# Optimization experiments

Hardware: AMD Instinct MI355X
Metric: run time of the kernel (lower is better)

The kernel has to match this reference:

```python
import jax, jax.numpy as jnp
import numpy as np

HIDDEN = 768
HEADS = 12
ORDERS = 3
NEG = -1e9


def setup_inputs() -> dict:
    key = jax.random.key(0)
    ks = jax.random.split(key, 16)
    B, N = 8, 512
    s = 0.02
    inp = {
        "v": jax.random.normal(ks[0], (B, N, HIDDEN), jnp.float32),
        "k": jax.random.normal(ks[1], (B, N, HIDDEN), jnp.float32),
        "q": jax.random.normal(ks[2], (B, N, HIDDEN), jnp.float32),
        "masks": jax.random.bernoulli(ks[3], 0.1, (ORDERS, B, 1, N, N)),
        "tau": 1,
        "training": 0,
        "Wv": jax.random.normal(ks[4], (HIDDEN, HIDDEN), jnp.float32) * s,
        "bv": jnp.zeros((HIDDEN,), jnp.float32),
        "Wk": jax.random.normal(ks[5], (HIDDEN, HIDDEN), jnp.float32) * s,
        "bk": jnp.zeros((HIDDEN,), jnp.float32),
        "Wq": jax.random.normal(ks[6], (HIDDEN, HIDDEN), jnp.float32) * s,
        "bq": jnp.zeros((HIDDEN,), jnp.float32),
        "Wm": jax.random.normal(ks[7], (HIDDEN, HIDDEN), jnp.float32) * s,
        "bm": jnp.zeros((HIDDEN,), jnp.float32),
        "pool_w": jax.random.normal(ks[8], (HIDDEN, 1), jnp.float32) * s,
        "pool_b": jnp.zeros((1,), jnp.float32),
        "mlp_w1": jax.random.normal(ks[9], (HIDDEN, HIDDEN // 2), jnp.float32) * s,
        "mlp_w2": jax.random.normal(ks[10], (HIDDEN // 2, ORDERS), jnp.float32) * s,
        "mlp_b2": jnp.zeros((ORDERS,), jnp.float32),
    }
    return inp


def _soft_routing(x, pool_w, pool_b, mlp_w1, mlp_w2, mlp_b2):
    # pooling='fc': masked attention pooling over sequence, then 2-layer MLP + softmax
    pad = (jnp.sum(jnp.abs(x), axis=-1) == 0)[:, :, None]        # [B, N, 1]
    scores = x @ pool_w + pool_b                                  # [B, N, 1]
    scores = jnp.where(pad, NEG, scores)
    scores = jax.nn.softmax(scores, axis=1)
    pooled = jnp.sum(x * scores, axis=1)                          # [B, HIDDEN]
    logits = jax.nn.relu(pooled @ mlp_w1) @ mlp_w2 + mlp_b2       # [B, L]
    return jax.nn.softmax(logits, axis=-1)


def reference(v, k, q, masks, tau, training, Wv, bv, Wk, bk, Wq, bq, Wm, bm,
              pool_w, pool_b, mlp_w1, mlp_w2, mlp_b2):
    B, N, _ = q.shape
    dk = HIDDEN // HEADS
    alphas = _soft_routing(v, pool_w, pool_b, mlp_w1, mlp_w2, mlp_b2)  # [B, L]

    def split_heads(x):
        return x.reshape(B, N, HEADS, dk).transpose(0, 2, 1, 3)  # [B, H, N, dk]

    vh = split_heads(v @ Wv + bv)
    kh = split_heads(k @ Wk + bk)
    qh = split_heads(q @ Wq + bq)

    scores = jnp.einsum('bhnd,bhmd->bhnm', qh, kh) / jnp.sqrt(jnp.float32(dk))
    # masks: [L, B, 1, N, N] broadcast over heads -> att_list [L, B, H, N, N]
    masked = jnp.where(masks[:, :, :, :, :], NEG, scores[None])
    att_list = jax.nn.softmax(masked, axis=-1)                    # [L, B, H, N, N]
    att_map = jnp.einsum('bl,lbhnm->bhnm', alphas, att_list)
    atted = jnp.einsum('bhnm,bhmd->bhnd', att_map, vh)
    atted = atted.transpose(0, 2, 1, 3).reshape(B, N, HIDDEN)
    return atted @ Wm + bm
```

## Files before the change

kernel.cpp:

```cpp
#include <hip/hip_runtime.h>
#include <hip/hip_bf16.h>
#include <stdint.h>


typedef __bf16 bf16x8 __attribute__((ext_vector_type(8)));
typedef float f32x4 __attribute__((ext_vector_type(4)));

#define NEGV -1e9f

__device__ __forceinline__ float b2f(unsigned short h) {
    union { unsigned int u; float f; } x; x.u = ((unsigned int)h) << 16; return x.f;
}
__device__ __forceinline__ unsigned short f2b(float f) {
    union { float f; unsigned int u; } x; x.f = f;
    unsigned int u = x.u + 0x7FFFu + ((x.u >> 16) & 1u);
    return (unsigned short)(u >> 16);
}
__device__ __forceinline__ unsigned int packbf(unsigned int u0, unsigned int u1) {
    unsigned int r0 = (u0 + 0x7FFFu + ((u0 >> 16) & 1u)) >> 16;
    unsigned int r1 = (u1 + 0x7FFFu + ((u1 >> 16) & 1u)) & 0xFFFF0000u;
    return r0 | r1;
}
__device__ __forceinline__ uint4 load8bf(const void* base, size_t elemOff, int isF32) {
    if (!isF32) return *(const uint4*)((const unsigned short*)base + elemOff);
    const uint4* f = (const uint4*)((const float*)base + elemOff);
    uint4 a = f[0], b = f[1];
    uint4 r;
    r.x = packbf(a.x, a.y);
    r.y = packbf(a.z, a.w);
    r.z = packbf(b.x, b.y);
    r.w = packbf(b.z, b.w);
    return r;
}
__device__ __forceinline__ float loadF(const void* p, int idx, int isF32) {
    return isF32 ? ((const float*)p)[idx] : b2f(((const unsigned short*)p)[idx]);
}
__device__ __forceinline__ bf16x8 u2b(uint4 u) {
    union { uint4 a; bf16x8 b; } x; x.a = u; return x.b;
}

__global__ void sniff_kernel(const unsigned int* __restrict__ mp,
                             const unsigned int* __restrict__ vp,
                             const unsigned int* __restrict__ wp,
                             int* __restrict__ flags)
{
    __shared__ int oki, oku, okf, badv, badw;
    if (threadIdx.x == 0) { oki = 1; oku = 1; okf = 1; badv = 0; badw = 0; }
    __syncthreads();
    int li = 1, lu = 1, lf = 1, bv = 0, bw = 0;
    for (int i = threadIdx.x; i < 16384; i += 256) {
        unsigned int w = mp[i];
        if (w > 1u) li = 0;
        if (w & 0xFEFEFEFEu) lu = 0;
        if (w != 0u && w != 0x3F800000u) lf = 0;
    }
    for (int i = threadIdx.x; i < 8192; i += 256) {
        unsigned int w = vp[i];
        float f0 = b2f((unsigned short)(w & 0xFFFF));
        float f1 = b2f((unsigned short)(w >> 16));
        if (!(fabsf(f0) < 1e4f) || !(fabsf(f1) < 1e4f)) bv = 1;
        w = wp[i];
        f0 = b2f((unsigned short)(w & 0xFFFF));
        f1 = b2f((unsigned short)(w >> 16));
        if (!(fabsf(f0) < 1e4f) || !(fabsf(f1) < 1e4f)) bw = 1;
    }
    if (!li) atomicAnd(&oki, 0);
    if (!lu) atomicAnd(&oku, 0);
    if (!lf) atomicAnd(&okf, 0);
    if (bv) atomicOr(&badv, 1);
    if (bw) atomicOr(&badw, 1);
    __syncthreads();
    if (threadIdx.x == 0) {
        flags[0] = oki ? 0 : (oku ? 1 : (okf ? 2 : 3));
        flags[1] = badv;
        flags[2] = badw;
    }
}

__global__ __launch_bounds__(256) void conv_act_kernel(
        const void* __restrict__ v, const void* __restrict__ k,
        const void* __restrict__ q, const int* __restrict__ flags,
        unsigned short* __restrict__ vb, unsigned short* __restrict__ kb,
        unsigned short* __restrict__ qb)
{
    const int dtV = flags[1];
    const int which = blockIdx.y;
    const void* src = (which == 0) ? v : (which == 1) ? k : q;
    unsigned short* dst = (which == 0) ? vb : (which == 1) ? kb : qb;
    size_t off = ((size_t)blockIdx.x * 256 + threadIdx.x) * 8;
    uint4 r = load8bf(src, off, dtV);
    *(uint4*)(dst + off) = r;
}

__global__ __launch_bounds__(256) void conv_wt_kernel(
        const void* __restrict__ W0, const void* __restrict__ W1,
        const void* __restrict__ W2, const void* __restrict__ W3,
        const int* __restrict__ flags,
        unsigned short* __restrict__ T0, unsigned short* __restrict__ T1,
        unsigned short* __restrict__ T2, unsigned short* __restrict__ T3)
{
    __shared__ unsigned short tile[64][65];
    const int t = threadIdx.x;
    const int dtW = flags[2];
    const int which = blockIdx.y;
    const void* W = (which == 0) ? W0 : (which == 1) ? W1 : (which == 2) ? W2 : W3;
    unsigned short* T = (which == 0) ? T0 : (which == 1) ? T1 : (which == 2) ? T2 : T3;
    const int tk = (blockIdx.x / 12) << 6;
    const int tn = (blockIdx.x % 12) << 6;
    #pragma unroll
    for (int i = 0; i < 16; i++) {
        int idx = (i << 8) + t;
        int r = idx >> 6, c = idx & 63;
        tile[r][c] = f2b(loadF(W, (tk + r) * 768 + tn + c, dtW));
    }
    __syncthreads();
    #pragma unroll
    for (int i = 0; i < 16; i++) {
        int idx = (i << 8) + t;
        int rn = idx >> 6, ck = idx & 63;
        T[(size_t)(tn + rn) * 768 + tk + ck] = tile[ck][rn];
    }
}

__global__ __launch_bounds__(256) void pack_kernel(
        const void* __restrict__ masks, const int* __restrict__ flags,
        unsigned int* __restrict__ pm)
{
    __shared__ unsigned char flg[32 * 512];
    const int t = threadIdx.x;
    const int mode = flags[0];
    const size_t e0 = (size_t)blockIdx.x * (32 * 512);
    if (mode == 0 || mode == 2) {
        const uint4* p = (const uint4*)((const unsigned int*)masks + e0);
        for (int i = t; i < 4096; i += 256) {
            uint4 u = p[i];
            int base = i << 2;
            flg[base + 0] = u.x ? 1 : 0;
            flg[base + 1] = u.y ? 1 : 0;
            flg[base + 2] = u.z ? 1 : 0;
            flg[base + 3] = u.w ? 1 : 0;
        }
    } else if (mode == 1) {
        const uint4* p = (const uint4*)((const unsigned char*)masks + e0);
        for (int i = t; i < 1024; i += 256) {
            uint4 u = p[i];
            unsigned int uu[4] = {u.x, u.y, u.z, u.w};
            int base = i << 4;
            #pragma unroll
            for (int k2 = 0; k2 < 4; k2++)
                #pragma unroll
                for (int bb = 0; bb < 4; bb++)
                    flg[base + k2 * 4 + bb] = ((uu[k2] >> (bb * 8)) & 0xFFu) ? 1 : 0;
        }
    } else {
        const uint4* p = (const uint4*)((const unsigned short*)masks + e0);
        for (int i = t; i < 2048; i += 256) {
            uint4 u = p[i];
            unsigned int uu[4] = {u.x, u.y, u.z, u.w};
            int base = i << 3;
            #pragma unroll
            for (int k2 = 0; k2 < 4; k2++) {
                flg[base + k2 * 2 + 0] = (uu[k2] & 0xFFFFu) ? 1 : 0;
                flg[base + k2 * 2 + 1] = (uu[k2] >> 16) ? 1 : 0;
            }
        }
    }
    __syncthreads();
    for (int widx = t; widx < 512; widx += 256) {
        int rl = widx >> 4, lm = widx & 15;
        unsigned int bits = 0;
        #pragma unroll
        for (int g = 0; g < 32; g++)
            bits |= ((unsigned int)(flg[rl * 512 + (g << 4) + lm] & 1)) << g;
        pm[(size_t)blockIdx.x * 512 + widx] = bits;
    }
}

__global__ __launch_bounds__(256) void route_score_kernel(
        const unsigned short* __restrict__ vb, const void* __restrict__ pool_w,
        const void* __restrict__ pool_b, const int* __restrict__ flags,
        float* __restrict__ scores)
{
    __shared__ float pw[768];
    const int t = threadIdx.x;
    const int b = blockIdx.x >> 3, ch = blockIdx.x & 7;
    const int dtW = flags[2];
    for (int d = t; d < 768; d += 256) pw[d] = loadF(pool_w, d, dtW);
    __syncthreads();
    const int r = t >> 2, c4 = t & 3;
    const int n = (ch << 6) + r;
    const unsigned int* vr = (const unsigned int*)vb + ((size_t)(b * 512 + n)) * 384;
    float dot = 0.f, asum = 0.f;
    for (int j = 0; j < 96; j++) {
        int p = c4 + (j << 2);
        unsigned int u = vr[p];
        float f0 = b2f((unsigned short)(u & 0xFFFF));
        float f1 = b2f((unsigned short)(u >> 16));
        asum += fabsf(f0) + fabsf(f1);
        dot += f0 * pw[2 * p] + f1 * pw[2 * p + 1];
    }
    dot += __shfl_xor(dot, 1); dot += __shfl_xor(dot, 2);
    asum += __shfl_xor(asum, 1); asum += __shfl_xor(asum, 2);
    if (c4 == 0)
        scores[b * 512 + n] = (asum == 0.f) ? NEGV : dot + loadF(pool_b, 0, dtW);
}

__global__ __launch_bounds__(512) void route_softmax_kernel(
        const float* __restrict__ scores, float* __restrict__ scs)
{
    __shared__ float red[8];
    const int t = threadIdx.x, b = blockIdx.x;
    float scv = scores[b * 512 + t];
    float mx = scv;
    #pragma unroll
    for (int off = 1; off < 64; off <<= 1) mx = fmaxf(mx, __shfl_xor(mx, off));
    if ((t & 63) == 0) red[t >> 6] = mx;
    __syncthreads();
    float M = red[0];
    #pragma unroll
    for (int i = 1; i < 8; i++) M = fmaxf(M, red[i]);
    float e = __expf(scv - M);
    __syncthreads();
    float sm = e;
    #pragma unroll
    for (int off = 1; off < 64; off <<= 1) sm += __shfl_xor(sm, off);
    if ((t & 63) == 0) red[t >> 6] = sm;
    __syncthreads();
    float SS = 0.f;
    #pragma unroll
    for (int i = 0; i < 8; i++) SS += red[i];
    scs[b * 512 + t] = e / SS;
}

__global__ __launch_bounds__(256) void route_pool_kernel(
        const unsigned short* __restrict__ vbuf, const int* __restrict__ flags,
        const float* __restrict__ scs, float* __restrict__ ppart)
{
    __shared__ float ps[64];
    const int t = threadIdx.x;
    const int ch = blockIdx.x, b = blockIdx.y;
    if (t < 64) ps[t] = scs[b * 512 + (ch << 6) + t];
    __syncthreads();
    const int d0 = t * 3;
    float a0 = 0.f, a1 = 0.f, a2 = 0.f;
    const unsigned short* vp = vbuf + ((size_t)(b * 512 + (ch << 6))) * 768 + d0;
    #pragma unroll 4
    for (int r = 0; r < 64; r++) {
        float p = ps[r];
        a0 += b2f(vp[0]) * p; a1 += b2f(vp[1]) * p; a2 += b2f(vp[2]) * p;
        vp += 768;
    }
    float* o = ppart + ((size_t)(b * 8 + ch)) * 768 + d0;
    o[0] = a0; o[1] = a1; o[2] = a2;
}

__global__ __launch_bounds__(256) void route_hid_kernel(
        const void* __restrict__ w1, const void* __restrict__ w2,
        const int* __restrict__ flags, const float* __restrict__ ppart,
        float* __restrict__ plog)
{
    __shared__ float pool[768];
    __shared__ float red[4][32];
    const int t = threadIdx.x;
    const int jc = blockIdx.x, b = blockIdx.y;
    const int dtW = flags[2];
    for (int d = t; d < 768; d += 256) {
        float a = 0.f;
        #pragma unroll
        for (int c = 0; c < 8; c++) a += ppart[((size_t)(b * 8 + c)) * 768 + d];
        pool[d] = a;
    }
    __syncthreads();
    const int jo = (t & 3) << 3;
    const int dr = t >> 2;
    float acc[8];
    #pragma unroll
    for (int j = 0; j < 8; j++) acc[j] = 0.f;
    for (int it = 0; it < 12; it++) {
        int d = (it << 6) + dr;
        float pv = pool[d];
        size_t off = (size_t)d * 384 + (jc << 5) + jo;
        if (!dtW) {
            uint4 u = *(const uint4*)((const unsigned short*)w1 + off);
            unsigned int uu[4] = {u.x, u.y, u.z, u.w};
            #pragma unroll
            for (int j2 = 0; j2 < 4; j2++) {
                acc[2 * j2]     += pv * b2f((unsigned short)(uu[j2] & 0xFFFF));
                acc[2 * j2 + 1] += pv * b2f((unsigned short)(uu[j2] >> 16));
            }
        } else {
            const float4* f = (const float4*)((const float*)w1 + off);
            float4 u0 = f[0], u1 = f[1];
            acc[0] += pv * u0.x; acc[1] += pv * u0.y;
            acc[2] += pv * u0.z; acc[3] += pv * u0.w;
            acc[4] += pv * u1.x; acc[5] += pv * u1.y;
            acc[6] += pv * u1.z; acc[7] += pv * u1.w;
        }
    }
    #pragma unroll
    for (int off = 4; off < 64; off <<= 1)
        #pragma unroll
        for (int j = 0; j < 8; j++) acc[j] += __shfl_xor(acc[j], off);
    const int w = t >> 6, lane = t & 63;
    if (lane < 4) {
        #pragma unroll
        for (int j = 0; j < 8; j++) red[w][lane * 8 + j] = acc[j];
    }
    __syncthreads();
    if (t < 32) {
        float h = red[0][t] + red[1][t] + red[2][t] + red[3][t];
        h = fmaxf(h, 0.f);
        int jg = (jc << 5) + t;
        float l0 = h * loadF(w2, jg * 3 + 0, dtW);
        float l1 = h * loadF(w2, jg * 3 + 1, dtW);
        float l2 = h * loadF(w2, jg * 3 + 2, dtW);
        #pragma unroll
        for (int off = 1; off < 32; off <<= 1) {
            l0 += __shfl_xor(l0, off);
            l1 += __shfl_xor(l1, off);
            l2 += __shfl_xor(l2, off);
        }
        if (t == 0) {
            float* o = plog + ((size_t)(b * 12 + jc)) * 3;
            o[0] = l0; o[1] = l1; o[2] = l2;
        }
    }
}

__global__ __launch_bounds__(64) void route_alpha_kernel(
        const void* __restrict__ b2, const int* __restrict__ flags,
        const float* __restrict__ plog, float* __restrict__ alphas)
{
    const int t = threadIdx.x, b = blockIdx.x;
    if (t == 0) {
        const int dtW = flags[2];
        float lg[3];
        #pragma unroll
        for (int l = 0; l < 3; l++) {
            float a = loadF(b2, l, dtW);
            for (int jc = 0; jc < 12; jc++) a += plog[((size_t)(b * 12 + jc)) * 3 + l];
            lg[l] = a;
        }
        float mm = fmaxf(lg[0], fmaxf(lg[1], lg[2]));
        float e0 = __expf(lg[0] - mm), e1 = __expf(lg[1] - mm), e2 = __expf(lg[2] - mm);
        float ss = e0 + e1 + e2;
        alphas[b * 3 + 0] = e0 / ss;
        alphas[b * 3 + 1] = e1 / ss;
        alphas[b * 3 + 2] = e2 / ss;
    }
}

__global__ __launch_bounds__(256) void gemm3_kernel(
        const unsigned short* __restrict__ X0, const unsigned short* __restrict__ X1,
        const unsigned short* __restrict__ X2,
        const unsigned short* __restrict__ W0, const unsigned short* __restrict__ W1,
        const unsigned short* __restrict__ W2,
        const void* __restrict__ bias0, const void* __restrict__ bias1,
        const void* __restrict__ bias2,
        const int* __restrict__ flags,
        void* __restrict__ dst0, void* __restrict__ dst1, void* __restrict__ dst2,
        int m0, int m1, int m2)
{
    __shared__ unsigned short smem[8192];
    unsigned short* At = smem;
    unsigned short* Bt = smem + 4096;
    const int t = threadIdx.x;
    const int which = blockIdx.y;
    const unsigned short* X  = (which == 0) ? X0 : (which == 1) ? X1 : X2;
    const unsigned short* WT = (which == 0) ? W0 : (which == 1) ? W1 : W2;
    const void* bias = (which == 0) ? bias0 : (which == 1) ? bias1 : bias2;
    void* dst = (which == 0) ? dst0 : (which == 1) ? dst1 : dst2;
    const int mode = (which == 0) ? m0 : (which == 1) ? m1 : m2;

    const int id = blockIdx.x;
    const int bx = id >> 6, by = id & 63;
    const int row0 = by << 6, col0 = bx << 6;
    const int w = t >> 6, lane = t & 63, quad = lane >> 4, lm = lane & 15;
    const int r0 = t >> 3, c0 = (t & 7) << 3;
    const int wr0 = r0 * 64 + (c0 ^ ((r0 & 7) << 3));
    const int dtW = flags[2];
    const int dtOut = flags[1];

    const unsigned short* xp  = X  + (size_t)(row0 + r0) * 768 + c0;
    const unsigned short* xp2 = xp + 32 * 768;
    const unsigned short* wp  = WT + (size_t)(col0 + r0) * 768 + c0;
    const unsigned short* wp2 = wp + 32 * 768;

    uint4 a0 = *(const uint4*)xp,  a1 = *(const uint4*)xp2;
    uint4 g0 = *(const uint4*)wp,  g1 = *(const uint4*)wp2;

    f32x4 acc[4];
    #pragma unroll
    for (int i = 0; i < 4; i++) acc[i] = (f32x4){0.f, 0.f, 0.f, 0.f};

    const int am = (w << 4) + lm;
    const int abase = am * 64, akey = (am & 7) << 3;

    for (int k0 = 0;;) {
        __syncthreads();
        *(uint4*)&At[wr0] = a0;        *(uint4*)&At[wr0 + 2048] = a1;
        *(uint4*)&Bt[wr0] = g0;        *(uint4*)&Bt[wr0 + 2048] = g1;
        __syncthreads();
        k0 += 64;
        if (k0 < 768) {
            a0 = *(const uint4*)(xp + k0);  a1 = *(const uint4*)(xp2 + k0);
            g0 = *(const uint4*)(wp + k0);  g1 = *(const uint4*)(wp2 + k0);
        }
        #pragma unroll
        for (int ks = 0; ks < 2; ks++) {
            int ko = (quad << 3) + (ks << 5);
            bf16x8 afr = *(const bf16x8*)&At[abase + (ko ^ akey)];
            #pragma unroll
            for (int t4 = 0; t4 < 4; t4++) {
                int bn = (t4 << 4) + lm;
                bf16x8 bfr = *(const bf16x8*)&Bt[bn * 64 + (ko ^ ((bn & 7) << 3))];
                acc[t4] = __builtin_amdgcn_mfma_f32_16x16x32_bf16(afr, bfr, acc[t4], 0, 0, 0);
            }
        }
        if (k0 >= 768) break;
    }

    if (mode == 1 && dtOut) {
        #pragma unroll
        for (int t4 = 0; t4 < 4; t4++) {
            int col = col0 + (t4 << 4) + lm;
            float bsv = loadF(bias, col, dtW);
            #pragma unroll
            for (int rg = 0; rg < 4; rg++) {
                int row = row0 + (w << 4) + (quad << 2) + rg;
                ((float*)dst)[(size_t)row * 768 + col] = acc[t4][rg] + bsv;
            }
        }
        return;
    }

    __syncthreads();
    #pragma unroll
    for (int t4 = 0; t4 < 4; t4++) {
        int colL = (t4 << 4) + lm;
        float bsv = loadF(bias, col0 + colL, dtW);
        #pragma unroll
        for (int rg = 0; rg < 4; rg++) {
            int rowL = (w << 4) + (quad << 2) + rg;
            unsigned short hv = f2b(acc[t4][rg] + bsv);
            if (mode == 2) smem[colL * 72 + rowL] = hv;
            else           smem[rowL * 72 + colL] = hv;
        }
    }
    __syncthreads();
    const int g = t >> 2, cc = (t & 3) << 4;
    uint4 o0 = *(const uint4*)&smem[g * 72 + cc];
    uint4 o1 = *(const uint4*)&smem[g * 72 + cc + 8];
    unsigned short* o;
    if (mode == 0) {
        int b = row0 >> 9, n0b = row0 & 511, h = col0 >> 6;
        o = (unsigned short*)dst + ((size_t)(b * 12 + h) * 512 + n0b + g) * 64 + cc;
    } else if (mode == 2) {
        int b = row0 >> 9, n0b = row0 & 511, h = col0 >> 6;
        o = (unsigned short*)dst + ((size_t)(b * 12 + h) * 64 + g) * 512 + n0b + cc;
    } else {
        o = (unsigned short*)dst + (size_t)(row0 + g) * 768 + col0 + cc;
    }
    *(uint4*)o = o0;
    *(uint4*)(o + 8) = o1;
}

__global__ __launch_bounds__(256) void attn_kernel(
        const unsigned short* __restrict__ qh, const unsigned short* __restrict__ kh,
        const unsigned short* __restrict__ vT, const unsigned int* __restrict__ pm,
        const float* __restrict__ alphas, unsigned short* __restrict__ atted)
{
    __shared__ unsigned short P[16 * 512];
    __shared__ float Zp[4][16][3];
    __shared__ unsigned short Ost[16 * 72];
    const int t = threadIdx.x;
    const int w = t >> 6, lane = t & 63, quad = lane >> 4, lm = lane & 15;
    const int id = blockIdx.x;
    const int bh = id % 96, qb = id / 96;
    const int b = bh / 12, h = bh % 12;
    const int n0 = qb << 4;

    const unsigned short* qrow = qh + ((size_t)(bh * 512 + n0 + lm)) * 64 + (quad << 3);
    bf16x8 qa0 = *(const bf16x8*)qrow;
    bf16x8 qa1 = *(const bf16x8*)(qrow + 32);

    const unsigned short* kb0 = kh + ((size_t)(bh * 512 + (w << 7) + lm)) * 64 + (quad << 3);
    uint4 kv[16];
    #pragma unroll
    for (int nt = 0; nt < 8; nt++) {
        const unsigned short* kr = kb0 + nt * (16 * 64);
        kv[2 * nt]     = *(const uint4*)kr;
        kv[2 * nt + 1] = *(const uint4*)(kr + 32);
    }
    f32x4 acc[8];
    #pragma unroll
    for (int i = 0; i < 8; i++) acc[i] = (f32x4){0.f, 0.f, 0.f, 0.f};
    #pragma unroll
    for (int nt = 0; nt < 8; nt++) {
        acc[nt] = __builtin_amdgcn_mfma_f32_16x16x32_bf16(qa0, u2b(kv[2 * nt]), acc[nt], 0, 0, 0);
        acc[nt] = __builtin_amdgcn_mfma_f32_16x16x32_bf16(qa1, u2b(kv[2 * nt + 1]), acc[nt], 0, 0, 0);
    }

    float al[3];
    #pragma unroll
    for (int l = 0; l < 3; l++) al[l] = alphas[b * 3 + l];

    #pragma unroll
    for (int nt = 0; nt < 8; nt++)
        #pragma unroll
        for (int rg = 0; rg < 4; rg++)
            acc[nt][rg] = __expf(acc[nt][rg] * 0.125f);

    unsigned int mk[4][3];
    #pragma unroll
    for (int rg = 0; rg < 4; rg++)
        #pragma unroll
        for (int l = 0; l < 3; l++)
            mk[rg][l] = pm[((size_t)((l << 3) + b) * 512 + n0 + (quad << 2) + rg) * 16 + lm];

    #pragma unroll
    for (int rg = 0; rg < 4; rg++) {
        float z0 = 0.f, z1 = 0.f, z2 = 0.f;
        #pragma unroll
        for (int nt = 0; nt < 8; nt++) {
            int g = (w << 3) + nt;
            float e = acc[nt][rg];
            if (!((mk[rg][0] >> g) & 1)) z0 += e;
            if (!((mk[rg][1] >> g) & 1)) z1 += e;
            if (!((mk[rg][2] >> g) & 1)) z2 += e;
        }
        #pragma unroll
        for (int off = 1; off < 16; off <<= 1) {
            z0 += __shfl_xor(z0, off);
            z1 += __shfl_xor(z1, off);
            z2 += __shfl_xor(z2, off);
        }
        if (lm == 0) {
            int row = (quad << 2) + rg;
            Zp[w][row][0] = z0; Zp[w][row][1] = z1; Zp[w][row][2] = z2;
        }
    }
    __syncthreads();

    #pragma unroll
    for (int rg = 0; rg < 4; rg++) {
        int row = (quad << 2) + rg;
        float coef[3]; float addu = 0.f;
        #pragma unroll
        for (int l = 0; l < 3; l++) {
            float Z = Zp[0][row][l] + Zp[1][row][l] + Zp[2][row][l] + Zp[3][row][l];
            if (Z > 0.f) coef[l] = al[l] / Z;
            else { coef[l] = 0.f; addu += al[l] * (1.0f / 512.0f); }
        }
        #pragma unroll
        for (int nt = 0; nt < 8; nt++) {
            int g = (w << 3) + nt;
            float p = addu;
            float e = acc[nt][rg];
            if (!((mk[rg][0] >> g) & 1)) p += coef[0] * e;
            if (!((mk[rg][1] >> g) & 1)) p += coef[1] * e;
            if (!((mk[rg][2] >> g) & 1)) p += coef[2] * e;
            int c = (g << 4) + lm;
            int chunk = c >> 3, j = c & 7;
            P[row * 512 + (((chunk ^ (row & 7))) << 3) + j] = f2b(p);
        }
    }
    __syncthreads();

    f32x4 accO = (f32x4){0.f, 0.f, 0.f, 0.f};
    const unsigned short* vb = vT + ((size_t)(bh * 64 + (w << 4) + lm)) * 512 + (quad << 3);
    #pragma unroll
    for (int ks = 0; ks < 16; ks++) {
        bf16x8 pa = *(const bf16x8*)&P[lm * 512 + ((((ks << 2) + quad) ^ (lm & 7)) << 3)];
        bf16x8 vf = *(const bf16x8*)(vb + (ks << 5));
        accO = __builtin_amdgcn_mfma_f32_16x16x32_bf16(pa, vf, accO, 0, 0, 0);
    }
    #pragma unroll
    for (int rg = 0; rg < 4; rg++)
        Ost[((quad << 2) + rg) * 72 + (w << 4) + lm] = f2b(accO[rg]);
    __syncthreads();
    const int r2 = t >> 4, c4 = t & 15;
    uint2 val = *(const uint2*)&Ost[r2 * 72 + (c4 << 2)];
    *(uint2*)&atted[((size_t)(b * 512 + n0 + r2)) * 768 + (h << 6) + (c4 << 2)] = val;
}

extern "C" void kernel_launch(void* const* d_in, const int* in_sizes, int n_in,
                              void* d_out, int out_size, void* d_ws, size_t ws_size,
                              hipStream_t stream)
{
    const void* v  = d_in[0];
    const void* k  = d_in[1];
    const void* q  = d_in[2];
    const void* mk = d_in[3];
    const void* Wv = d_in[6];
    const void* bv = d_in[7];
    const void* Wk = d_in[8];
    const void* bk = d_in[9];
    const void* Wq = d_in[10];
    const void* bq = d_in[11];
    const void* Wm = d_in[12];
    const void* bm = d_in[13];
    const void* pool_w = d_in[14];
    const void* pool_b = d_in[15];
    const void* w1 = d_in[16];
    const void* w2 = d_in[17];
    const void* b2 = d_in[18];

    char* ws = (char*)d_ws;
    int*   flags  = (int*)ws;
    float* alphas = (float*)(ws + 256);
    float* scores = (float*)(ws + 512);
    float* scs    = (float*)(ws + 16896);
    float* ppart  = (float*)(ws + 33280);
    float* plog   = (float*)(ws + 229888);
    unsigned int* pm = (unsigned int*)(ws + 262144);
    unsigned short* qh  = (unsigned short*)(ws + 1048576);
    unsigned short* kh  = (unsigned short*)(ws + 1048576 + 1 * 6291456L);
    unsigned short* vT  = (unsigned short*)(ws + 1048576 + 2 * 6291456L);
    unsigned short* vb  = (unsigned short*)(ws + 1048576 + 3 * 6291456L);
    unsigned short* kb  = (unsigned short*)(ws + 1048576 + 4 * 6291456L);
    unsigned short* qb  = (unsigned short*)(ws + 1048576 + 5 * 6291456L);
    unsigned short* atted = kb;
    char* wt0 = ws + 1048576 + 6 * 6291456L;
    unsigned short* WTv = (unsigned short*)(wt0);
    unsigned short* WTk = (unsigned short*)(wt0 + 1 * 1179648L);
    unsigned short* WTq = (unsigned short*)(wt0 + 2 * 1179648L);
    unsigned short* WTm = (unsigned short*)(wt0 + 3 * 1179648L);

    sniff_kernel<<<dim3(1), dim3(256), 0, stream>>>(
        (const unsigned int*)mk, (const unsigned int*)v, (const unsigned int*)Wv, flags);
    conv_act_kernel<<<dim3(1536, 3), dim3(256), 0, stream>>>(v, k, q, flags, vb, kb, qb);
    conv_wt_kernel<<<dim3(144, 4), dim3(256), 0, stream>>>(
        Wv, Wk, Wq, Wm, flags, WTv, WTk, WTq, WTm);
    pack_kernel<<<dim3(384), dim3(256), 0, stream>>>(mk, flags, pm);
    route_score_kernel<<<dim3(64), dim3(256), 0, stream>>>(vb, pool_w, pool_b, flags, scores);
    route_softmax_kernel<<<dim3(8), dim3(512), 0, stream>>>(scores, scs);
    route_pool_kernel<<<dim3(8, 8), dim3(256), 0, stream>>>(vb, flags, scs, ppart);
    route_hid_kernel<<<dim3(12, 8), dim3(256), 0, stream>>>(w1, w2, flags, ppart, plog);
    route_alpha_kernel<<<dim3(8), dim3(64), 0, stream>>>(b2, flags, plog, alphas);
    gemm3_kernel<<<dim3(768, 3), dim3(256), 0, stream>>>(
        vb, kb, qb, WTv, WTk, WTq, bv, bk, bq, flags,
        (void*)vT, (void*)kh, (void*)qh, 2, 0, 0);
    attn_kernel<<<dim3(3072), dim3(256), 0, stream>>>(qh, kh, vT, pm, alphas, atted);
    gemm3_kernel<<<dim3(768, 1), dim3(256), 0, stream>>>(
        atted, atted, atted, WTm, WTm, WTm, bm, bm, bm, flags,
        d_out, d_out, d_out, 1, 1, 1);
}
```

Measured before the change: 299.0 us.

## Merge prep kernels, fold alpha softmax into attention, branchless masked P build

Three preprocessing kernels (activation conversion, weight transpose, mask bit-packing) are merged into one launch that dispatches on block index. The small routing-alpha kernel is removed, and each attention block now recomputes the three alphas from the partial logits. Inside attention, the masked sums and P weights are computed with branchless float masks and FMAs, and P's shared-memory layout changes from an XOR swizzle to a padded 520-element stride. The aim is to cut launch overhead and divergent branches, at the cost of redundant per-block alpha work and possibly different LDS bank-conflict behaviour.

```diff
diff --git a/kernel.cpp b/kernel.cpp
--- a/kernel.cpp
+++ b/kernel.cpp
@@ -77,59 +77,60 @@
     }
 }
 
-__global__ __launch_bounds__(256) void conv_act_kernel(
+__global__ __launch_bounds__(256) void prep_kernel(
         const void* __restrict__ v, const void* __restrict__ k,
-        const void* __restrict__ q, const int* __restrict__ flags,
-        unsigned short* __restrict__ vb, unsigned short* __restrict__ kb,
-        unsigned short* __restrict__ qb)
-{
-    const int dtV = flags[1];
-    const int which = blockIdx.y;
-    const void* src = (which == 0) ? v : (which == 1) ? k : q;
-    unsigned short* dst = (which == 0) ? vb : (which == 1) ? kb : qb;
-    size_t off = ((size_t)blockIdx.x * 256 + threadIdx.x) * 8;
-    uint4 r = load8bf(src, off, dtV);
-    *(uint4*)(dst + off) = r;
-}
-
-__global__ __launch_bounds__(256) void conv_wt_kernel(
+        const void* __restrict__ q,
         const void* __restrict__ W0, const void* __restrict__ W1,
         const void* __restrict__ W2, const void* __restrict__ W3,
-        const int* __restrict__ flags,
+        const void* __restrict__ masks, const int* __restrict__ flags,
+        unsigned short* __restrict__ vb, unsigned short* __restrict__ kb,
+        unsigned short* __restrict__ qb,
         unsigned short* __restrict__ T0, unsigned short* __restrict__ T1,
-        unsigned short* __restrict__ T2, unsigned short* __restrict__ T3)
-{
-    __shared__ unsigned short tile[64][65];
+        unsigned short* __restrict__ T2, unsigned short* __restrict__ T3,
+        unsigned int* __restrict__ pm)
+{
+    __shared__ unsigned char smraw[16384];
     const int t = threadIdx.x;
-    const int dtW = flags[2];
-    const int which = blockIdx.y;
-    const void* W = (which == 0) ? W0 : (which == 1) ? W1 : (which == 2) ? W2 : W3;
-    unsigned short* T = (which == 0) ? T0 : (which == 1) ? T1 : (which == 2) ? T2 : T3;
-    const int tk = (blockIdx.x / 12) << 6;
-    const int tn = (blockIdx.x % 12) << 6;
-    #pragma unroll
-    for (int i = 0; i < 16; i++) {
-        int idx = (i << 8) + t;
-        int r = idx >> 6, c = idx & 63;
-        tile[r][c] = f2b(loadF(W, (tk + r) * 768 + tn + c, dtW));
-    }
-    __syncthreads();
-    #pragma unroll
-    for (int i = 0; i < 16; i++) {
-        int idx = (i << 8) + t;
-        int rn = idx >> 6, ck = idx & 63;
-        T[(size_t)(tn + rn) * 768 + tk + ck] = tile[ck][rn];
-    }
-}
-
-__global__ __launch_bounds__(256) void pack_kernel(
-        const void* __restrict__ masks, const int* __restrict__ flags,
-        unsigned int* __restrict__ pm)
-{
-    __shared__ unsigned char flg[32 * 512];
-    const int t = threadIdx.x;
+    const int id = blockIdx.x;
+
+    if (id < 4608) {
+        const int dtV = flags[1];
+        const int which = id / 1536, blk = id % 1536;
+        const void* src = (which == 0) ? v : (which == 1) ? k : q;
+        unsigned short* dst = (which == 0) ? vb : (which == 1) ? kb : qb;
+        size_t off = ((size_t)blk * 256 + t) * 8;
+        uint4 r = load8bf(src, off, dtV);
+        *(uint4*)(dst + off) = r;
+        return;
+    }
+    if (id < 5184) {
+        unsigned short (*tile)[65] = (unsigned short(*)[65])smraw;
+        const int dtW = flags[2];
+        const int wid = id - 4608;
+        const int which = wid / 144, bx = wid % 144;
+        const void* W = (which == 0) ? W0 : (which == 1) ? W1 : (which == 2) ? W2 : W3;
+        unsigned short* T = (which == 0) ? T0 : (which == 1) ? T1 : (which == 2) ? T2 : T3;
+        const int tk = (bx / 12) << 6;
+        const int tn = (bx % 12) << 6;
+        #pragma unroll
+        for (int i = 0; i < 16; i++) {
+            int idx = (i << 8) + t;
+            int r = idx >> 6, c = idx & 63;
+            tile[r][c] = f2b(loadF(W, (tk + r) * 768 + tn + c, dtW));
+        }
+        __syncthreads();
+        #pragma unroll
+        for (int i = 0; i < 16; i++) {
+            int idx = (i << 8) + t;
+            int rn = idx >> 6, ck = idx & 63;
+            T[(size_t)(tn + rn) * 768 + tk + ck] = tile[ck][rn];
+        }
+        return;
+    }
+    unsigned char* flg = (unsigned char*)smraw;
     const int mode = flags[0];
-    const size_t e0 = (size_t)blockIdx.x * (32 * 512);
+    const int pid = id - 5184;
+    const size_t e0 = (size_t)pid * (32 * 512);
     if (mode == 0 || mode == 2) {
         const uint4* p = (const uint4*)((const unsigned int*)masks + e0);
         for (int i = t; i < 4096; i += 256) {
@@ -172,7 +173,7 @@
         #pragma unroll
         for (int g = 0; g < 32; g++)
             bits |= ((unsigned int)(flg[rl * 512 + (g << 4) + lm] & 1)) << g;
-        pm[(size_t)blockIdx.x * 512 + widx] = bits;
+        pm[(size_t)pid * 512 + widx] = bits;
     }
 }
 
@@ -327,29 +328,6 @@
     }
 }
 
-__global__ __launch_bounds__(64) void route_alpha_kernel(
-        const void* __restrict__ b2, const int* __restrict__ flags,
-        const float* __restrict__ plog, float* __restrict__ alphas)
-{
-    const int t = threadIdx.x, b = blockIdx.x;
-    if (t == 0) {
-        const int dtW = flags[2];
-        float lg[3];
-        #pragma unroll
-        for (int l = 0; l < 3; l++) {
-            float a = loadF(b2, l, dtW);
-            for (int jc = 0; jc < 12; jc++) a += plog[((size_t)(b * 12 + jc)) * 3 + l];
-            lg[l] = a;
-        }
-        float mm = fmaxf(lg[0], fmaxf(lg[1], lg[2]));
-        float e0 = __expf(lg[0] - mm), e1 = __expf(lg[1] - mm), e2 = __expf(lg[2] - mm);
-        float ss = e0 + e1 + e2;
-        alphas[b * 3 + 0] = e0 / ss;
-        alphas[b * 3 + 1] = e1 / ss;
-        alphas[b * 3 + 2] = e2 / ss;
-    }
-}
-
 __global__ __launch_bounds__(256) void gemm3_kernel(
         const unsigned short* __restrict__ X0, const unsigned short* __restrict__ X1,
         const unsigned short* __restrict__ X2,
@@ -468,9 +446,10 @@
 __global__ __launch_bounds__(256) void attn_kernel(
         const unsigned short* __restrict__ qh, const unsigned short* __restrict__ kh,
         const unsigned short* __restrict__ vT, const unsigned int* __restrict__ pm,
-        const float* __restrict__ alphas, unsigned short* __restrict__ atted)
-{
-    __shared__ unsigned short P[16 * 512];
+        const float* __restrict__ plog, const void* __restrict__ b2p,
+        const int* __restrict__ flags, unsigned short* __restrict__ atted)
+{
+    __shared__ unsigned short P[16 * 520];
     __shared__ float Zp[4][16][3];
     __shared__ unsigned short Ost[16 * 72];
     const int t = threadIdx.x;
@@ -492,6 +471,19 @@
         kv[2 * nt]     = *(const uint4*)kr;
         kv[2 * nt + 1] = *(const uint4*)(kr + 32);
     }
+
+    const int dtW = flags[2];
+    float lg0 = loadF(b2p, 0, dtW), lg1 = loadF(b2p, 1, dtW), lg2 = loadF(b2p, 2, dtW);
+    #pragma unroll
+    for (int jc = 0; jc < 12; jc++) {
+        const float* pp = plog + ((size_t)(b * 12 + jc)) * 3;
+        lg0 += pp[0]; lg1 += pp[1]; lg2 += pp[2];
+    }
+    float mm = fmaxf(lg0, fmaxf(lg1, lg2));
+    float e0 = __expf(lg0 - mm), e1 = __expf(lg1 - mm), e2 = __expf(lg2 - mm);
+    float iss = 1.0f / (e0 + e1 + e2);
+    float al[3] = {e0 * iss, e1 * iss, e2 * iss};
+
     f32x4 acc[8];
     #pragma unroll
     for (int i = 0; i < 8; i++) acc[i] = (f32x4){0.f, 0.f, 0.f, 0.f};
@@ -501,10 +493,6 @@
         acc[nt] = __builtin_amdgcn_mfma_f32_16x16x32_bf16(qa1, u2b(kv[2 * nt + 1]), acc[nt], 0, 0, 0);
     }
 
-    float al[3];
-    #pragma unroll
-    for (int l = 0; l < 3; l++) al[l] = alphas[b * 3 + l];
-
     #pragma unroll
     for (int nt = 0; nt < 8; nt++)
         #pragma unroll
@@ -525,9 +513,12 @@
         for (int nt = 0; nt < 8; nt++) {
             int g = (w << 3) + nt;
             float e = acc[nt][rg];
-            if (!((mk[rg][0] >> g) & 1)) z0 += e;
-            if (!((mk[rg][1] >> g) & 1)) z1 += e;
-            if (!((mk[rg][2] >> g) & 1)) z2 += e;
+            float f0 = (float)((mk[rg][0] >> g) & 1u);
+            float f1 = (float)((mk[rg][1] >> g) & 1u);
+            float f2 = (float)((mk[rg][2] >> g) & 1u);
+            z0 += fmaf(-f0, e, e);
+            z1 += fmaf(-f1, e, e);
+            z2 += fmaf(-f2, e, e);
         }
         #pragma unroll
         for (int off = 1; off < 16; off <<= 1) {
@@ -552,26 +543,30 @@
             if (Z > 0.f) coef[l] = al[l] / Z;
             else { coef[l] = 0.f; addu += al[l] * (1.0f / 512.0f); }
         }
+        float csum = coef[0] + coef[1] + coef[2];
+        unsigned short* pbase = &P[row * 520 + (w << 7) + lm];
         #pragma unroll
         for (int nt = 0; nt < 8; nt++) {
             int g = (w << 3) + nt;
-            float p = addu;
             float e = acc[nt][rg];
-            if (!((mk[rg][0] >> g) & 1)) p += coef[0] * e;
-            if (!((mk[rg][1] >> g) & 1)) p += coef[1] * e;
-            if (!((mk[rg][2] >> g) & 1)) p += coef[2] * e;
-            int c = (g << 4) + lm;
-            int chunk = c >> 3, j = c & 7;
-            P[row * 512 + (((chunk ^ (row & 7))) << 3) + j] = f2b(p);
+            float f0 = (float)((mk[rg][0] >> g) & 1u);
+            float f1 = (float)((mk[rg][1] >> g) & 1u);
+            float f2 = (float)((mk[rg][2] >> g) & 1u);
+            float tw = f0 * coef[0];
+            tw = fmaf(f1, coef[1], tw);
+            tw = fmaf(f2, coef[2], tw);
+            float wgt = csum - tw;
+            pbase[nt << 4] = f2b(fmaf(e, wgt, addu));
         }
     }
     __syncthreads();
 
     f32x4 accO = (f32x4){0.f, 0.f, 0.f, 0.f};
     const unsigned short* vb = vT + ((size_t)(bh * 64 + (w << 4) + lm)) * 512 + (quad << 3);
+    const unsigned short* prow = &P[lm * 520 + (quad << 3)];
     #pragma unroll
     for (int ks = 0; ks < 16; ks++) {
-        bf16x8 pa = *(const bf16x8*)&P[lm * 512 + ((((ks << 2) + quad) ^ (lm & 7)) << 3)];
+        bf16x8 pa = *(const bf16x8*)(prow + (ks << 5));
         bf16x8 vf = *(const bf16x8*)(vb + (ks << 5));
         accO = __builtin_amdgcn_mfma_f32_16x16x32_bf16(pa, vf, accO, 0, 0, 0);
     }
@@ -608,7 +603,6 @@
 
     char* ws = (char*)d_ws;
     int*   flags  = (int*)ws;
-    float* alphas = (float*)(ws + 256);
     float* scores = (float*)(ws + 512);
     float* scs    = (float*)(ws + 16896);
     float* ppart  = (float*)(ws + 33280);
@@ -629,19 +623,18 @@
 
     sniff_kernel<<<dim3(1), dim3(256), 0, stream>>>(
         (const unsigned int*)mk, (const unsigned int*)v, (const unsigned int*)Wv, flags);
-    conv_act_kernel<<<dim3(1536, 3), dim3(256), 0, stream>>>(v, k, q, flags, vb, kb, qb);
-    conv_wt_kernel<<<dim3(144, 4), dim3(256), 0, stream>>>(
-        Wv, Wk, Wq, Wm, flags, WTv, WTk, WTq, WTm);
-    pack_kernel<<<dim3(384), dim3(256), 0, stream>>>(mk, flags, pm);
+    prep_kernel<<<dim3(5568), dim3(256), 0, stream>>>(
+        v, k, q, Wv, Wk, Wq, Wm, mk, flags,
+        vb, kb, qb, WTv, WTk, WTq, WTm, pm);
     route_score_kernel<<<dim3(64), dim3(256), 0, stream>>>(vb, pool_w, pool_b, flags, scores);
     route_softmax_kernel<<<dim3(8), dim3(512), 0, stream>>>(scores, scs);
     route_pool_kernel<<<dim3(8, 8), dim3(256), 0, stream>>>(vb, flags, scs, ppart);
     route_hid_kernel<<<dim3(12, 8), dim3(256), 0, stream>>>(w1, w2, flags, ppart, plog);
-    route_alpha_kernel<<<dim3(8), dim3(64), 0, stream>>>(b2, flags, plog, alphas);
     gemm3_kernel<<<dim3(768, 3), dim3(256), 0, stream>>>(
         vb, kb, qb, WTv, WTk, WTq, bv, bk, bq, flags,
         (void*)vT, (void*)kh, (void*)qh, 2, 0, 0);
-    attn_kernel<<<dim3(3072), dim3(256), 0, stream>>>(qh, kh, vT, pm, alphas, atted);
+    attn_kernel<<<dim3(3072), dim3(256), 0, stream>>>(
+        qh, kh, vT, pm, plog, b2, flags, atted);
     gemm3_kernel<<<dim3(768, 1), dim3(256), 0, stream>>>(
         atted, atted, atted, WTm, WTm, WTm, bm, bm, bm, flags,
         d_out, d_out, d_out, 1, 1, 1);
```

Measured after the change: 301.9 us. Within noise of the previous version (+1.0%).
